# Kernel tuning notes

Measured on AMD Instinct MI355X. Metric: run time of the kernel, lower is better.

The kernel has to match this reference:

```python
import jax, jax.numpy as jnp
import numpy as np

DIM = 512
CODEBOOK_SIZE = 2048
NUM_Q = 8
COMMIT_W = 0.25
B, T = 8, 2048


def setup_inputs() -> dict:
    key = jax.random.key(0)
    k1, k2 = jax.random.split(key)
    x = jax.random.normal(k1, (B, T, DIM), dtype=jnp.float32)
    lim = 1.0 / CODEBOOK_SIZE
    codebooks = jax.random.uniform(k2, (NUM_Q, CODEBOOK_SIZE, DIM), dtype=jnp.float32,
                                   minval=-lim, maxval=lim)
    return {"x": x, "codebooks": codebooks}


def reference(x, codebooks):
    """Residual VQ forward.
    x: (B, T, D); codebooks: (Q, K, D).
    Returns (quantized (B,T,D), indices (B,T,Q) int32, mean loss scalar).
    """
    sg = jax.lax.stop_gradient
    residual = x
    quantized = jnp.zeros_like(x)
    idx_list = []
    total_loss = jnp.zeros((), dtype=x.dtype)
    for i in range(NUM_Q):
        cb = codebooks[i]  # (K, D)
        # squared L2 distances: (B,T,K)
        d = (jnp.sum(residual * residual, axis=-1, keepdims=True)
             - 2.0 * jnp.einsum('btd,kd->btk', residual, cb)
             + jnp.sum(cb * cb, axis=-1))
        min_idx = jnp.argmin(d, axis=-1)  # (B,T)
        idx_list.append(min_idx)
        q_lvl = cb[min_idx]  # (B,T,D) gather
        quantized = quantized + q_lvl
        commit_loss = jnp.mean((sg(residual) - q_lvl) ** 2)
        codebook_loss = jnp.mean((residual - sg(q_lvl)) ** 2)
        total_loss = total_loss + commit_loss * COMMIT_W + codebook_loss
        residual = residual - sg(q_lvl)
    # straight-through estimator
    quantized = x + sg(quantized - x)
    indices = jnp.stack(idx_list, axis=-1)  # (B,T,Q)
    return quantized, indices, total_loss / NUM_Q
```

## Files before the change

### kernel.cpp

```cpp
#include <hip/hip_runtime.h>


constexpr int DIM   = 512;
constexpr int KCB   = 2048;
constexpr int NQ    = 8;
constexpr int NTOK  = 8 * 2048;
constexpr int QELEM = NTOK * DIM;
constexpr int NBLK  = KCB / 128;
constexpr float WINDOW = 1e-3f;

using short8  = __attribute__((ext_vector_type(8))) short;
using float4v = __attribute__((ext_vector_type(4))) float;

__device__ __forceinline__ unsigned short f2bf(float f) {
    unsigned u = __float_as_uint(f);
    return (unsigned short)((u + 0x7FFFu + ((u >> 16) & 1u)) >> 16);
}

__device__ __forceinline__ void gl2lds16(const void* g, void* l) {
    __builtin_amdgcn_global_load_lds(
        (__attribute__((address_space(1))) void*)g,
        (__attribute__((address_space(3))) void*)l, 16, 0, 0);
}

struct Top4 { float s[4]; int i[4]; };
__device__ __forceinline__ void t4_init(Top4& t) {
#pragma unroll
    for (int j = 0; j < 4; ++j) { t.s[j] = 3.0e38f; t.i[j] = 0x7FFFFFFF; }
}
__device__ __forceinline__ void t4_ins(Top4& t, float s, int idx) {
    if (s < t.s[3]) {
        if (s < t.s[2]) { t.s[3] = t.s[2]; t.i[3] = t.i[2];
            if (s < t.s[1]) { t.s[2] = t.s[1]; t.i[2] = t.i[1];
                if (s < t.s[0]) { t.s[1] = t.s[0]; t.i[1] = t.i[0]; t.s[0] = s; t.i[0] = idx; }
                else            { t.s[1] = s; t.i[1] = idx; }
            } else { t.s[2] = s; t.i[2] = idx; }
        } else { t.s[3] = s; t.i[3] = idx; }
    }
}

__global__ void k_initcvt(const float4* __restrict__ x, const float4* __restrict__ cbs,
                          float4* __restrict__ R, ushort4* __restrict__ Rb,
                          ushort4* __restrict__ Cbb)
{
    int i = blockIdx.x * blockDim.x + threadIdx.x;
    constexpr int N4 = QELEM / 4;
    if (i < N4) {
        float4 v = x[i];
        R[i] = v;
        Rb[i] = make_ushort4(f2bf(v.x), f2bf(v.y), f2bf(v.z), f2bf(v.w));
    } else {
        int j = i - N4;
        float4 v = cbs[j];
        Cbb[j] = make_ushort4(f2bf(v.x), f2bf(v.y), f2bf(v.z), f2bf(v.w));
    }
}

__global__ __launch_bounds__(256) void k_sqnorm_np(const float* __restrict__ A,
                                                   float* __restrict__ out)
{
#pragma clang fp contract(off)
    __shared__ float buf[4][DIM];
    __shared__ float accs[4][32];
    const int w = threadIdx.x >> 6, lane = threadIdx.x & 63;
    const int row = blockIdx.x * 4 + w;

    const float4* a4 = reinterpret_cast<const float4*>(A + (size_t)row * DIM);
    float4* b4 = reinterpret_cast<float4*>(buf[w]);
    b4[lane]      = a4[lane];
    b4[lane + 64] = a4[lane + 64];
    __syncthreads();
    if (lane < 32) {
        int blk = lane >> 3, j = lane & 7;
        const float* p = buf[w] + blk * 128 + j;
        float x0 = p[0];
        float acc = x0 * x0;
#pragma unroll
        for (int m = 1; m < 16; ++m) { float x = p[8 * m]; acc = acc + x * x; }
        accs[w][lane] = acc;
    }
    __syncthreads();
    if (lane == 0) {
        float B[4];
#pragma unroll
        for (int blk = 0; blk < 4; ++blk) {
            const float* r = &accs[w][blk * 8];
            B[blk] = ((r[0] + r[1]) + (r[2] + r[3])) + ((r[4] + r[5]) + (r[6] + r[7]));
        }
        out[row] = (B[0] + B[1]) + (B[2] + B[3]);
    }
}

__global__ __launch_bounds__(256, 3) void k_gemm_topk(
        const unsigned short* __restrict__ Rb, const unsigned short* __restrict__ Cbb,
        const float* __restrict__ c2, float* __restrict__ candS, int* __restrict__ candI)
{
    __shared__ __align__(16) char smem[49664];
    unsigned short* A0 = (unsigned short*)smem;
    unsigned short* B0 = (unsigned short*)(smem + 24576);
    float*  scb = (float*)smem;
    float*  c2s = (float*)(smem + 49152);

    const int tid  = threadIdx.x;
    const int wid  = tid >> 6, lane = tid & 63;
    const int quad = lane >> 4, l16 = lane & 15;

    const int L    = blockIdx.y * NBLK + blockIdx.x;
    const int slot = L >> 3;
    const int mb   = (L & 7) * 16 + (slot >> 4);
    const int nb   = slot & 15;

    const int tok0 = mb * 128, n0 = nb * 128;
    const int nw = (wid & 1) * 64;
    const int fbA = (wid >> 1) * 4;
    const int fbB = (wid & 1) * 4;

    if (tid < 128) c2s[tid] = c2[n0 + tid];

    float4v acc[4][4];
    float4v zero = {0.f, 0.f, 0.f, 0.f};
#pragma unroll
    for (int mi = 0; mi < 4; ++mi)
#pragma unroll
        for (int nj = 0; nj < 4; ++nj) acc[mi][nj] = zero;

    auto stage = [&](int b, int kb) {
        unsigned short* Ad = A0 + b * 4096;
        unsigned short* Bd = B0 + b * 4096;
#pragma unroll
        for (int i = 0; i < 2; ++i) {
            int mi_abs = i * 4 + wid;
            gl2lds16(&Rb[(size_t)(tok0 + mi_abs * 16 + l16) * DIM + kb + quad * 8],
                     Ad + (size_t)(i * 256 + wid * 64) * 8);
            gl2lds16(&Cbb[(size_t)(n0 + mi_abs * 16 + l16) * DIM + kb + quad * 8],
                     Bd + (size_t)(i * 256 + wid * 64) * 8);
        }
    };

    auto compute = [&](int b) {
        const unsigned short* Ac = A0 + b * 4096;
        const unsigned short* Bc = B0 + b * 4096;
        short8 af[4], bf[4];
#pragma unroll
        for (int mi = 0; mi < 4; ++mi)
            af[mi] = *(const short8*)(Ac + ((size_t)(fbA + mi) * 64 + lane) * 8);
#pragma unroll
        for (int nj = 0; nj < 4; ++nj)
            bf[nj] = *(const short8*)(Bc + ((size_t)(fbB + nj) * 64 + lane) * 8);
#pragma unroll
        for (int mi = 0; mi < 4; ++mi)
#pragma unroll
            for (int nj = 0; nj < 4; ++nj)
                acc[mi][nj] = __builtin_amdgcn_mfma_f32_16x16x32_bf16(
                    af[mi], bf[nj], acc[mi][nj], 0, 0, 0);
    };

    stage(0, 0);
    stage(1, 32);
    int cur = 0, pf = 2;
    for (int it = 0; it < 15; ++it) {
        asm volatile("s_waitcnt vmcnt(4)" ::: "memory");
        __builtin_amdgcn_s_barrier();
        __builtin_amdgcn_sched_barrier(0);
        if (it < 14) stage(pf, (it + 2) * 32);
        compute(cur);
        cur = (cur == 2) ? 0 : cur + 1;
        pf  = (pf  == 2) ? 0 : pf  + 1;
    }
    asm volatile("s_waitcnt vmcnt(0)" ::: "memory");
    __builtin_amdgcn_s_barrier();
    __builtin_amdgcn_sched_barrier(0);
    compute(cur);

    for (int h = 0; h < 2; ++h) {
        __syncthreads();
        if ((wid >> 1) == h) {
#pragma unroll
            for (int mi = 0; mi < 4; ++mi)
#pragma unroll
                for (int nj = 0; nj < 4; ++nj) {
                    int r0 = mi * 16 + quad * 4;
                    int cc = nw + nj * 16 + l16;
#pragma unroll
                    for (int e = 0; e < 4; ++e)
                        scb[(r0 + e) * 132 + cc] = acc[mi][nj][e];
                }
        }
        __syncthreads();
        int row = tid >> 2, part = tid & 3;
        Top4 t; t4_init(t);
#pragma unroll
        for (int i = 0; i < 32; ++i) {
            int col = part + 4 * i;
            float s = c2s[col] - 2.0f * scb[row * 132 + col];
            t4_ins(t, s, n0 + col);
        }
#pragma unroll
        for (int k = 1; k <= 2; k <<= 1) {
            float os[4]; int oi[4];
#pragma unroll
            for (int j = 0; j < 4; ++j) {
                os[j] = __shfl_xor(t.s[j], k, 64);
                oi[j] = __shfl_xor(t.i[j], k, 64);
            }
#pragma unroll
            for (int j = 0; j < 4; ++j) t4_ins(t, os[j], oi[j]);
        }
        if (part == 0) {
            int token = tok0 + h * 64 + row;
            size_t base = (size_t)token * 64 + (size_t)nb * 4;
#pragma unroll
            for (int j = 0; j < 4; ++j) { candS[base + j] = t.s[j]; candI[base + j] = t.i[j]; }
        }
    }
}

__global__ __launch_bounds__(256) void k_selupd(
        const float* __restrict__ candS, const int* __restrict__ candI,
        float* __restrict__ R, const float* __restrict__ cbf,
        float* __restrict__ r2, const float* __restrict__ c2,
        float* __restrict__ idx_out, float* __restrict__ partial,
        ushort4* __restrict__ Rb, const float4* __restrict__ x, int level)
{
#pragma clang fp contract(off)
    __shared__ float buf[4][DIM];
    __shared__ float accs[4][32];
    __shared__ float shl[4];
    const int w = threadIdx.x >> 6, lane = threadIdx.x & 63;
    const int t = blockIdx.x * 4 + w;
    const bool last = (level == NQ - 1);

    float4* r4 = reinterpret_cast<float4*>(R + (size_t)t * DIM);
    float4* b4 = reinterpret_cast<float4*>(buf[w]);
    float4 rr[2];
    rr[0] = r4[lane];      rr[1] = r4[lane + 64];
    b4[lane] = rr[0];      b4[lane + 64] = rr[1];

    float sb = candS[(size_t)t * 64 + lane];
    int   ci = candI[(size_t)t * 64 + lane];
    float mn = sb;
#pragma unroll
    for (int off = 32; off; off >>= 1) mn = fminf(mn, __shfl_xor(mn, off, 64));
    unsigned long long mask = __ballot(sb <= mn + WINDOW);
    int ncand = __popcll(mask);
    int winner;
    if (ncand == 1) {
        winner = __shfl(ci, __ffsll(mask) - 1, 64);
    } else {
        int src = 0;
        if (lane < ncand) {
            unsigned long long mm = mask;
            for (int z = 0; z < lane; ++z) mm &= mm - 1;
            src = __ffsll(mm) - 1;
        }
        int cidx = __shfl(ci, src, 64);
        float s = 3.0e38f;
        int   si = 0x7FFFFFFF;
        if (lane < ncand) {
            const float4* cp4 = reinterpret_cast<const float4*>(cbf + (size_t)cidx * DIM);
            const float4* rp4 = reinterpret_cast<const float4*>(buf[w]);
            float d = 0.f;
#pragma unroll 4
            for (int j = 0; j < DIM / 4; ++j) {
                float4 cv = cp4[j];
                float4 rv = rp4[j];
                d = fmaf(rv.x, cv.x, d);
                d = fmaf(rv.y, cv.y, d);
                d = fmaf(rv.z, cv.z, d);
                d = fmaf(rv.w, cv.w, d);
            }
            float td = 2.0f * d;
            float a  = r2[t] - td;
            s  = a + c2[cidx];
            si = cidx;
        }
#pragma unroll
        for (int off = 32; off; off >>= 1) {
            float ov = __shfl_xor(s, off, 64);
            int   oi = __shfl_xor(si, off, 64);
            if (ov < s || (ov == s && oi < si)) { s = ov; si = oi; }
        }
        winner = si;
    }
    if (lane == 0) idx_out[(size_t)t * NQ + level] = (float)winner;

    const float4* c4 = reinterpret_cast<const float4*>(cbf + (size_t)winner * DIM);
    float ls = 0.f;
#pragma unroll
    for (int i = 0; i < 2; ++i) {
        int d = lane + 64 * i;
        float4 rv = rr[i], cv = c4[d];
        rv.x -= cv.x; rv.y -= cv.y; rv.z -= cv.z; rv.w -= cv.w;
        ls = ls + rv.x * rv.x; ls = ls + rv.y * rv.y;
        ls = ls + rv.z * rv.z; ls = ls + rv.w * rv.w;
        if (!last) {
            r4[d] = rv;
            b4[d] = rv;
            Rb[(size_t)t * 128 + d] = make_ushort4(f2bf(rv.x), f2bf(rv.y),
                                                   f2bf(rv.z), f2bf(rv.w));
        } else {
            float4 xv = x[(size_t)t * 128 + d];
            xv.x -= rv.x; xv.y -= rv.y; xv.z -= rv.z; xv.w -= rv.w;
            r4[d] = xv;
        }
    }

    if (!last) {
        __syncthreads();
        if (lane < 32) {
            int blk = lane >> 3, j = lane & 7;
            const float* p = buf[w] + blk * 128 + j;
            float x0 = p[0];
            float acc = x0 * x0;
#pragma unroll
            for (int m = 1; m < 16; ++m) { float xx = p[8 * m]; acc = acc + xx * xx; }
            accs[w][lane] = acc;
        }
        __syncthreads();
        if (lane == 0) {
            float B[4];
#pragma unroll
            for (int blk = 0; blk < 4; ++blk) {
                const float* r = &accs[w][blk * 8];
                B[blk] = ((r[0] + r[1]) + (r[2] + r[3])) + ((r[4] + r[5]) + (r[6] + r[7]));
            }
            r2[t] = (B[0] + B[1]) + (B[2] + B[3]);
        }
    }

#pragma unroll
    for (int off = 32; off; off >>= 1) ls += __shfl_down(ls, off, 64);
    if (lane == 0) shl[w] = ls;
    __syncthreads();
    if (threadIdx.x == 0) partial[blockIdx.x] = (shl[0] + shl[1]) + (shl[2] + shl[3]);
}

__global__ __launch_bounds__(256) void k_finalize_loss(const float* __restrict__ partial,
                                                       float* __restrict__ loss_out)
{
    double s = 0.0;
    for (int i = threadIdx.x; i < NQ * (NTOK / 4); i += 256) s += (double)partial[i];
#pragma unroll
    for (int off = 32; off; off >>= 1) s += __shfl_down(s, off, 64);
    __shared__ double sh[4];
    if ((threadIdx.x & 63) == 0) sh[threadIdx.x >> 6] = s;
    __syncthreads();
    if (threadIdx.x == 0) {
        double tot = (sh[0] + sh[1]) + (sh[2] + sh[3]);
        loss_out[0] = (float)(tot * 1.25 / ((double)NQ * (double)QELEM));
    }
}

extern "C" void kernel_launch(void* const* d_in, const int* in_sizes, int n_in,
                              void* d_out, int out_size, void* d_ws, size_t ws_size,
                              hipStream_t stream)
{
    const float* x   = (const float*)d_in[0];
    const float* cbs = (const float*)d_in[1];

    float* qout     = (float*)d_out;
    float* idx_out  = qout + QELEM;
    float* loss_out = idx_out + (size_t)NTOK * NQ;
    float* R        = qout;

    char* ws = (char*)d_ws;
    size_t off = 0;
    unsigned short* Rb   = (unsigned short*)(ws + off); off += (size_t)QELEM * 2;
    unsigned short* Cbb  = (unsigned short*)(ws + off); off += (size_t)QELEM * 2;
    float*          c2   = (float*)(ws + off);          off += (size_t)NQ * KCB * 4;
    float*          r2   = (float*)(ws + off);          off += (size_t)NTOK * 4;
    float*          part = (float*)(ws + off);          off += (size_t)NQ * (NTOK / 4) * 4;
    float*          candS= (float*)(ws + off);          off += (size_t)NTOK * 64 * 4;
    int*            candI= (int*)(ws + off);            off += (size_t)NTOK * 64 * 4;

    k_initcvt<<<2 * (QELEM / 4) / 256, 256, 0, stream>>>((const float4*)x, (const float4*)cbs,
                                                         (float4*)R, (ushort4*)Rb,
                                                         (ushort4*)Cbb);
    k_sqnorm_np<<<NQ * KCB / 4, 256, 0, stream>>>(cbs, c2);
    k_sqnorm_np<<<NTOK / 4, 256, 0, stream>>>(R, r2);

    for (int q = 0; q < NQ; ++q) {
        const float*          cbq  = cbs + (size_t)q * KCB * DIM;
        const unsigned short* cbbq = Cbb + (size_t)q * KCB * DIM;
        const float*          c2q  = c2 + (size_t)q * KCB;
        dim3 g(NBLK, NTOK / 128);
        k_gemm_topk<<<g, 256, 0, stream>>>(Rb, cbbq, c2q, candS, candI);
        k_selupd<<<NTOK / 4, 256, 0, stream>>>(candS, candI, R, cbq, r2, c2q,
                                               idx_out, part + (size_t)q * (NTOK / 4),
                                               (ushort4*)Rb, (const float4*)x, q);
    }

    k_finalize_loss<<<1, 256, 0, stream>>>(part, loss_out);
}
```

Baseline: 1.041 ms.

## Fuse init conversion with norm kernels, raise MFMA priority, vectorize top-k scan

Merges the fp32-to-bf16 conversion and the two squared-norm kernels into one launch that reads x and the codebooks only once. In the GEMM kernel, the MFMA block is wrapped in s_setprio so compute waves get issue priority. The top-k epilogue now scans columns in contiguous float4 chunks and keeps c2 in registers instead of doing strided scalar LDS reads. The contiguous ordering changes which columns each lane handles, though the final top-4 merge should give the same candidates.

New measurement: 1.006 ms. 1.04x faster.

```diff
diff --git a/kernel.cpp b/kernel.cpp
--- a/kernel.cpp
+++ b/kernel.cpp
@@ -39,36 +39,37 @@
     }
 }
 
-__global__ void k_initcvt(const float4* __restrict__ x, const float4* __restrict__ cbs,
-                          float4* __restrict__ R, ushort4* __restrict__ Rb,
-                          ushort4* __restrict__ Cbb)
-{
-    int i = blockIdx.x * blockDim.x + threadIdx.x;
-    constexpr int N4 = QELEM / 4;
-    if (i < N4) {
-        float4 v = x[i];
-        R[i] = v;
-        Rb[i] = make_ushort4(f2bf(v.x), f2bf(v.y), f2bf(v.z), f2bf(v.w));
-    } else {
-        int j = i - N4;
-        float4 v = cbs[j];
-        Cbb[j] = make_ushort4(f2bf(v.x), f2bf(v.y), f2bf(v.z), f2bf(v.w));
-    }
-}
-
-__global__ __launch_bounds__(256) void k_sqnorm_np(const float* __restrict__ A,
-                                                   float* __restrict__ out)
+__global__ __launch_bounds__(256) void k_initnorm(
+        const float* __restrict__ x, const float* __restrict__ cbs,
+        float4* __restrict__ R, ushort4* __restrict__ Rb, ushort4* __restrict__ Cbb,
+        float* __restrict__ r2, float* __restrict__ c2)
 {
 #pragma clang fp contract(off)
     __shared__ float buf[4][DIM];
     __shared__ float accs[4][32];
     const int w = threadIdx.x >> 6, lane = threadIdx.x & 63;
-    const int row = blockIdx.x * 4 + w;
-
-    const float4* a4 = reinterpret_cast<const float4*>(A + (size_t)row * DIM);
+    const bool isX = blockIdx.x < (NTOK / 4);
+    const int row = (isX ? blockIdx.x : blockIdx.x - NTOK / 4) * 4 + w;
+
+    const float* src = isX ? x : cbs;
+    const float4* a4 = reinterpret_cast<const float4*>(src + (size_t)row * DIM);
+    float4 v0 = a4[lane], v1 = a4[lane + 64];
+
+    ushort4 b0 = make_ushort4(f2bf(v0.x), f2bf(v0.y), f2bf(v0.z), f2bf(v0.w));
+    ushort4 b1 = make_ushort4(f2bf(v1.x), f2bf(v1.y), f2bf(v1.z), f2bf(v1.w));
+    if (isX) {
+        R [(size_t)row * 128 + lane]      = v0;
+        R [(size_t)row * 128 + lane + 64] = v1;
+        Rb[(size_t)row * 128 + lane]      = b0;
+        Rb[(size_t)row * 128 + lane + 64] = b1;
+    } else {
+        Cbb[(size_t)row * 128 + lane]      = b0;
+        Cbb[(size_t)row * 128 + lane + 64] = b1;
+    }
+
     float4* b4 = reinterpret_cast<float4*>(buf[w]);
-    b4[lane]      = a4[lane];
-    b4[lane + 64] = a4[lane + 64];
+    b4[lane]      = v0;
+    b4[lane + 64] = v1;
     __syncthreads();
     if (lane < 32) {
         int blk = lane >> 3, j = lane & 7;
@@ -76,7 +77,7 @@
         float x0 = p[0];
         float acc = x0 * x0;
 #pragma unroll
-        for (int m = 1; m < 16; ++m) { float x = p[8 * m]; acc = acc + x * x; }
+        for (int m = 1; m < 16; ++m) { float xx = p[8 * m]; acc = acc + xx * xx; }
         accs[w][lane] = acc;
     }
     __syncthreads();
@@ -87,7 +88,8 @@
             const float* r = &accs[w][blk * 8];
             B[blk] = ((r[0] + r[1]) + (r[2] + r[3])) + ((r[4] + r[5]) + (r[6] + r[7]));
         }
-        out[row] = (B[0] + B[1]) + (B[2] + B[3]);
+        float out = (B[0] + B[1]) + (B[2] + B[3]);
+        if (isX) r2[row] = out; else c2[row] = out;
     }
 }
 
@@ -147,12 +149,14 @@
 #pragma unroll
         for (int nj = 0; nj < 4; ++nj)
             bf[nj] = *(const short8*)(Bc + ((size_t)(fbB + nj) * 64 + lane) * 8);
+        __builtin_amdgcn_s_setprio(1);
 #pragma unroll
         for (int mi = 0; mi < 4; ++mi)
 #pragma unroll
             for (int nj = 0; nj < 4; ++nj)
                 acc[mi][nj] = __builtin_amdgcn_mfma_f32_16x16x32_bf16(
                     af[mi], bf[nj], acc[mi][nj], 0, 0, 0);
+        __builtin_amdgcn_s_setprio(0);
     };
 
     stage(0, 0);
@@ -172,6 +176,12 @@
     __builtin_amdgcn_sched_barrier(0);
     compute(cur);
 
+    const int row_ = tid >> 2, part_ = tid & 3;
+    float4 c2r[8];
+#pragma unroll
+    for (int j = 0; j < 8; ++j)
+        c2r[j] = *(const float4*)(c2s + part_ * 32 + 4 * j);
+
     for (int h = 0; h < 2; ++h) {
         __syncthreads();
         if ((wid >> 1) == h) {
@@ -187,13 +197,16 @@
                 }
         }
         __syncthreads();
-        int row = tid >> 2, part = tid & 3;
         Top4 t; t4_init(t);
 #pragma unroll
-        for (int i = 0; i < 32; ++i) {
-            int col = part + 4 * i;
-            float s = c2s[col] - 2.0f * scb[row * 132 + col];
-            t4_ins(t, s, n0 + col);
+        for (int j = 0; j < 8; ++j) {
+            float4 sv = *(const float4*)(scb + row_ * 132 + part_ * 32 + 4 * j);
+            float4 cv = c2r[j];
+            int c0 = n0 + part_ * 32 + 4 * j;
+            t4_ins(t, cv.x - 2.0f * sv.x, c0 + 0);
+            t4_ins(t, cv.y - 2.0f * sv.y, c0 + 1);
+            t4_ins(t, cv.z - 2.0f * sv.z, c0 + 2);
+            t4_ins(t, cv.w - 2.0f * sv.w, c0 + 3);
         }
 #pragma unroll
         for (int k = 1; k <= 2; k <<= 1) {
@@ -206,8 +219,8 @@
 #pragma unroll
             for (int j = 0; j < 4; ++j) t4_ins(t, os[j], oi[j]);
         }
-        if (part == 0) {
-            int token = tok0 + h * 64 + row;
+        if (part_ == 0) {
+            int token = tok0 + h * 64 + row_;
             size_t base = (size_t)token * 64 + (size_t)nb * 4;
 #pragma unroll
             for (int j = 0; j < 4; ++j) { candS[base + j] = t.s[j]; candI[base + j] = t.i[j]; }
@@ -373,11 +386,8 @@
     float*          candS= (float*)(ws + off);          off += (size_t)NTOK * 64 * 4;
     int*            candI= (int*)(ws + off);            off += (size_t)NTOK * 64 * 4;
 
-    k_initcvt<<<2 * (QELEM / 4) / 256, 256, 0, stream>>>((const float4*)x, (const float4*)cbs,
-                                                         (float4*)R, (ushort4*)Rb,
-                                                         (ushort4*)Cbb);
-    k_sqnorm_np<<<NQ * KCB / 4, 256, 0, stream>>>(cbs, c2);
-    k_sqnorm_np<<<NTOK / 4, 256, 0, stream>>>(R, r2);
+    k_initnorm<<<NTOK / 4 + NQ * KCB / 4, 256, 0, stream>>>(
+        x, cbs, (float4*)R, (ushort4*)Rb, (ushort4*)Cbb, r2, c2);
 
     for (int q = 0; q < NQ; ++q) {
         const float*          cbq  = cbs + (size_t)q * KCB * DIM;
```
